# Optimization experiments

Measured on AMD Instinct MI355X. Metric: run time of the kernel, lower is better.

Reference implementation:

```python
import jax, jax.numpy as jnp
import numpy as np

HIDDEN = 1024
HEADS = 16
HEAD = HIDDEN // HEADS
B, S = 4, 2048


def setup_inputs() -> dict:
    key = jax.random.key(0)
    ks = jax.random.split(key, 12)
    sc = 1.0 / np.sqrt(HIDDEN)
    return {
        "query": jax.random.normal(ks[0], (B, S, HIDDEN), jnp.float32),
        "key_in": jax.random.normal(ks[1], (B, S, HIDDEN), jnp.float32),
        "value": jax.random.normal(ks[2], (B, S, HIDDEN), jnp.float32),
        "mask": jax.random.randint(ks[3], (B, S, S), 0, 2, jnp.int32),
        "w_q": jax.random.uniform(ks[4], (HIDDEN, HIDDEN), jnp.float32, -sc, sc),
        "b_q": jax.random.uniform(ks[5], (HIDDEN,), jnp.float32, -sc, sc),
        "w_k": jax.random.uniform(ks[6], (HIDDEN, HIDDEN), jnp.float32, -sc, sc),
        "b_k": jax.random.uniform(ks[7], (HIDDEN,), jnp.float32, -sc, sc),
        "w_v": jax.random.uniform(ks[8], (HIDDEN, HIDDEN), jnp.float32, -sc, sc),
        "b_v": jax.random.uniform(ks[9], (HIDDEN,), jnp.float32, -sc, sc),
    }


def _split_heads(x):
    # [B, S, H*D] -> [B, H, S, D]
    b, s, _ = x.shape
    return x.reshape(b, s, HEADS, HEAD).transpose(0, 2, 1, 3)


def reference(query, key_in, value, mask, w_q, b_q, w_k, b_k, w_v, b_v):
    # torch Linear: x @ W.T + b
    Q = _split_heads(query @ w_q.T + b_q)
    K = _split_heads(key_in @ w_k.T + b_k)
    V = _split_heads(value @ w_v.T + b_v)
    scale = 1.0 / np.sqrt(HEAD).astype(np.float32)
    scores = jnp.einsum("bhqd,bhkd->bhqk", Q, K) * scale
    # mask broadcast over heads; masked_fill where mask == 0
    scores = jnp.where(mask[:, None, :, :] == 0, jnp.float32(-1e9), scores)
    attn = jax.nn.softmax(scores, axis=-1)
    ctx = jnp.einsum("bhqk,bhkd->bhqd", attn, V)
    ctx = ctx.transpose(0, 2, 1, 3).reshape(query.shape[0], -1, HIDDEN)
    return (ctx, attn)
```

## Files before the change

kernel.cpp:

```cpp
#include <hip/hip_runtime.h>
#include <hip/hip_bf16.h>
#include <cstdint>
#include <cstddef>

typedef __attribute__((ext_vector_type(4)))  float f32x4;
typedef __attribute__((ext_vector_type(8)))  short s16x8;
typedef __attribute__((ext_vector_type(8)))  unsigned short u16x8;
typedef __attribute__((ext_vector_type(4)))  unsigned short u16x4;
typedef unsigned short ushort_t;
typedef unsigned long long u64;

#define MFMA_BF16(a, b, c) __builtin_amdgcn_mfma_f32_16x16x32_bf16((a), (b), (c), 0, 0, 0)

constexpr int BATCH  = 4;
constexpr int SEQ    = 2048;
constexpr int NHEAD  = 16;
constexpr int HEADD  = 64;
constexpr int HID    = 1024;
constexpr int BH     = BATCH * NHEAD;

#define QSCALE 0.180336880091961f

__device__ __forceinline__ ushort_t f2bf(float f) {
  return __builtin_bit_cast(ushort_t, __float2bfloat16(f));
}

__device__ __forceinline__ int ps_off(int q, int k) {
  return q * 136 + ((((k >> 3) ^ ((q >> 3) & 7)) & 15) << 3) + (k & 7);
}

__global__ __launch_bounds__(256, 2) void proj_fused_kernel(
    const float* __restrict__ q_in, const float* __restrict__ k_in,
    const float* __restrict__ v_in,
    const float* __restrict__ w_q, const float* __restrict__ b_q,
    const float* __restrict__ w_k, const float* __restrict__ b_k,
    const float* __restrict__ w_v, const float* __restrict__ b_v,
    ushort_t* __restrict__ Qp, ushort_t* __restrict__ Kp,
    ushort_t* __restrict__ Vp,
    const int* __restrict__ mask, u64* __restrict__ pm) {
  const int z = blockIdx.z;
  if (z == 3) {
    const int nwords = BATCH * SEQ * SEQ / 64;
    const int lane = threadIdx.x & 63;
    int wid = (blockIdx.y * gridDim.x + blockIdx.x) * 4 + (threadIdx.x >> 6);
    const int step = gridDim.x * gridDim.y * 4;
    for (; wid < nwords; wid += step) {
      int mv = __builtin_nontemporal_load(mask + (size_t)wid * 64 + lane);
      u64 bits = __ballot(mv != 0);
      if (lane == 0) pm[wid] = bits;
    }
    return;
  }
  const float* X    = (z == 0) ? q_in : (z == 1) ? k_in : v_in;
  const float* W    = (z == 0) ? w_q : (z == 1) ? w_k : w_v;
  const float* bias = (z == 0) ? b_q : (z == 1) ? b_k : b_v;
  const float scale = (z == 0) ? QSCALE : 1.0f;

  __shared__ ushort_t As[128 * 72];
  __shared__ ushort_t Bs[128 * 72];
  const int tid  = threadIdx.x;
  const int lane = tid & 63;
  const int wave = tid >> 6;
  const int wr = wave >> 1, wc = wave & 1;
  const int lo = lane & 15, hi = lane >> 4;
  const int mb = blockIdx.y, nb = blockIdx.x;

  const int srow = tid >> 4;
  const int scol = (tid & 15) * 4;

  f32x4 acc[4][4];
#pragma unroll
  for (int i = 0; i < 4; i++)
#pragma unroll
    for (int j = 0; j < 4; j++) acc[i][j] = (f32x4){0.f, 0.f, 0.f, 0.f};

  const float* xa = X + (size_t)(mb * 128 + srow) * HID + scol;
  const float* xb = W + (size_t)(nb * 128 + srow) * HID + scol;

  for (int k0 = 0; k0 < HID; k0 += 64) {
#pragma unroll
    for (int rr = 0; rr < 128; rr += 16) {
      float4 av = *(const float4*)(xa + (size_t)rr * HID + k0);
      float4 bv = *(const float4*)(xb + (size_t)rr * HID + k0);
      u16x4 a4 = {f2bf(av.x), f2bf(av.y), f2bf(av.z), f2bf(av.w)};
      u16x4 b4 = {f2bf(bv.x), f2bf(bv.y), f2bf(bv.z), f2bf(bv.w)};
      *(u16x4*)(&As[(srow + rr) * 72 + scol]) = a4;
      *(u16x4*)(&Bs[(srow + rr) * 72 + scol]) = b4;
    }
    __syncthreads();
#pragma unroll
    for (int kk = 0; kk < 2; kk++) {
      const int ko = kk * 32 + hi * 8;
      s16x8 af[4], bf[4];
#pragma unroll
      for (int i = 0; i < 4; i++)
        af[i] = *(const s16x8*)(&As[(wr * 64 + i * 16 + lo) * 72 + ko]);
#pragma unroll
      for (int j = 0; j < 4; j++)
        bf[j] = *(const s16x8*)(&Bs[(wc * 64 + j * 16 + lo) * 72 + ko]);
#pragma unroll
      for (int i = 0; i < 4; i++)
#pragma unroll
        for (int j = 0; j < 4; j++)
          acc[i][j] = MFMA_BF16(af[i], bf[j], acc[i][j]);
    }
    __syncthreads();
  }
  if (z != 2) {
    ushort_t* out = (z == 0) ? Qp : Kp;
#pragma unroll
    for (int j = 0; j < 4; j++) {
      const int n = nb * 128 + wc * 64 + j * 16 + lo;
      const float bvn = bias[n];
      const int h = n >> 6, d = n & 63;
#pragma unroll
      for (int i = 0; i < 4; i++) {
        const int m0 = mb * 128 + wr * 64 + i * 16 + hi * 4;
#pragma unroll
        for (int r = 0; r < 4; r++) {
          const int m = m0 + r;
          const int b = m >> 11, s = m & 2047;
          float v = (acc[i][j][r] + bvn) * scale;
          __builtin_nontemporal_store(
              f2bf(v), out + (((size_t)(b * NHEAD + h) * SEQ) + s) * HEADD + d);
        }
      }
    }
  } else {
#pragma unroll
    for (int j = 0; j < 4; j++) {
      const int n = nb * 128 + wc * 64 + j * 16 + lo;
      const float bvn = bias[n];
      const int h = n >> 6, d = n & 63;
#pragma unroll
      for (int i = 0; i < 4; i++) {
        const int m0 = mb * 128 + wr * 64 + i * 16 + hi * 4;
        const int b = m0 >> 11, s0 = m0 & 2047;
        u16x4 pk = {f2bf(acc[i][j][0] + bvn), f2bf(acc[i][j][1] + bvn),
                    f2bf(acc[i][j][2] + bvn), f2bf(acc[i][j][3] + bvn)};
        __builtin_nontemporal_store(
            pk, (u16x4*)(Vp + ((size_t)(b * NHEAD + h) * HEADD + d) * SEQ + s0));
      }
    }
  }
}

__global__ __launch_bounds__(256, 2) void fused_attn_kernel(
    const ushort_t* __restrict__ Qp, const ushort_t* __restrict__ Kp,
    const ushort_t* __restrict__ Vtg, const u64* __restrict__ pm,
    float* __restrict__ attn, float* __restrict__ ctx) {
  extern __shared__ ushort_t smem[];
  ushort_t* Vt = smem;
  ushort_t* Ps = smem + 8704;

  const int tid  = threadIdx.x;
  const int lane = tid & 63, wave = tid >> 6;
  const int lo = lane & 15, hi = lane >> 4;

  const int f   = blockIdx.x;
  const int xcd = f & 7, i5 = f >> 3;
  const int bh  = xcd * 8 + (i5 & 7);
  const int qb  = i5 >> 3;
  const int b = bh >> 4, h = bh & 15;

  const ushort_t* Qg = Qp + ((size_t)bh * SEQ + qb * 128 + wave * 32) * HEADD;
  s16x8 aq[2][2];
#pragma unroll
  for (int i = 0; i < 2; i++)
#pragma unroll
    for (int kk = 0; kk < 2; kk++)
      aq[i][kk] = *(const s16x8*)(Qg + (size_t)(i * 16 + lo) * HEADD + kk * 32 + hi * 8);

  const ushort_t* Kg = Kp + (size_t)bh * SEQ * HEADD;
  const ushort_t* Vg = Vtg + (size_t)bh * HEADD * SEQ;
  const u64* pmb = pm + (size_t)b * SEQ * 32;
  const int q0 = qb * 128 + wave * 32;

  float lrun[2][4];
#pragma unroll
  for (int i = 0; i < 2; i++)
#pragma unroll
    for (int r = 0; r < 4; r++) lrun[i][r] = 0.f;
  f32x4 pacc[2][4];
#pragma unroll
  for (int i = 0; i < 2; i++)
#pragma unroll
    for (int jd = 0; jd < 4; jd++) pacc[i][jd] = (f32x4){0.f, 0.f, 0.f, 0.f};

  const int vr16 = tid >> 4;
  const int vc8  = (tid & 15) * 8;

  for (int kt = 0; kt < SEQ / 128; kt++) {
    u16x8 vreg[4];
#pragma unroll
    for (int it = 0; it < 4; it++)
      vreg[it] = *(const u16x8*)(Vg + (size_t)(it * 16 + vr16) * SEQ + kt * 128 + vc8);

    f32x4 sacc[2][8];
#pragma unroll
    for (int i = 0; i < 2; i++)
#pragma unroll
      for (int j = 0; j < 8; j++) sacc[i][j] = (f32x4){0.f, 0.f, 0.f, 0.f};
#pragma unroll
    for (int j = 0; j < 8; j++) {
      const ushort_t* kr = Kg + (size_t)(kt * 128 + j * 16 + lo) * HEADD + hi * 8;
      s16x8 b0 = *(const s16x8*)(kr);
      s16x8 b1 = *(const s16x8*)(kr + 32);
      sacc[0][j] = MFMA_BF16(aq[0][0], b0, sacc[0][j]);
      sacc[1][j] = MFMA_BF16(aq[1][0], b0, sacc[1][j]);
      sacc[0][j] = MFMA_BF16(aq[0][1], b1, sacc[0][j]);
      sacc[1][j] = MFMA_BF16(aq[1][1], b1, sacc[1][j]);
    }

#pragma unroll
    for (int it = 0; it < 4; it++)
      *(u16x8*)(&Vt[(it * 16 + vr16) * 136 + vc8]) = vreg[it];

#pragma unroll
    for (int i = 0; i < 2; i++)
#pragma unroll
      for (int r = 0; r < 4; r++) {
        const int q = q0 + i * 16 + hi * 4 + r;
        const u64* pw = pmb + (size_t)q * 32 + kt * 2;
        u64 s0 = pw[0] >> lo, s1 = pw[1] >> lo;
        const int prow = wave * 32 + i * 16 + hi * 4 + r;
        float tsum = 0.f;
#pragma unroll
        for (int j = 0; j < 8; j++) {
          unsigned bit = (unsigned)((j < 4 ? (s0 >> (j * 16)) : (s1 >> ((j - 4) * 16))) & 1ull);
          float s = bit ? sacc[i][j][r] : -1e30f;
          float ev = __builtin_amdgcn_exp2f(s);
          tsum += ev;
          Ps[ps_off(prow, j * 16 + lo)] = f2bf(ev);
        }
        lrun[i][r] += tsum;
      }
    __syncthreads();

#pragma unroll
    for (int kkp = 0; kkp < 4; kkp++) {
      const int ko = kkp * 32 + hi * 8;
      s16x8 ap0 = *(const s16x8*)(&Ps[ps_off(wave * 32 + lo, ko)]);
      s16x8 ap1 = *(const s16x8*)(&Ps[ps_off(wave * 32 + 16 + lo, ko)]);
#pragma unroll
      for (int jd = 0; jd < 4; jd++) {
        s16x8 bv = *(const s16x8*)(&Vt[(jd * 16 + lo) * 136 + ko]);
        pacc[0][jd] = MFMA_BF16(ap0, bv, pacc[0][jd]);
        pacc[1][jd] = MFMA_BF16(ap1, bv, pacc[1][jd]);
      }
    }
    __syncthreads();
  }

  float il[2][4], mi[2][4];
#pragma unroll
  for (int i = 0; i < 2; i++)
#pragma unroll
    for (int r = 0; r < 4; r++) {
      float l = lrun[i][r];
#pragma unroll
      for (int off = 1; off < 16; off <<= 1) l += __shfl_xor(l, off);
      il[i][r] = 1.0f / l;
      mi[i][r] = __builtin_amdgcn_logf(l);
    }
#pragma unroll
  for (int i = 0; i < 2; i++)
#pragma unroll
    for (int jd = 0; jd < 4; jd++)
#pragma unroll
      for (int r = 0; r < 4; r++) {
        const int q = q0 + i * 16 + hi * 4 + r;
        __builtin_nontemporal_store(
            pacc[i][jd][r] * il[i][r],
            ctx + ((size_t)b * SEQ + q) * HID + h * HEADD + jd * 16 + lo);
      }

  for (int kt = 0; kt < SEQ / 128; kt++) {
    f32x4 sacc[2][8];
#pragma unroll
    for (int i = 0; i < 2; i++)
#pragma unroll
      for (int j = 0; j < 8; j++) sacc[i][j] = (f32x4){0.f, 0.f, 0.f, 0.f};
#pragma unroll
    for (int j = 0; j < 8; j++) {
      const ushort_t* kr = Kg + (size_t)(kt * 128 + j * 16 + lo) * HEADD + hi * 8;
      s16x8 b0 = *(const s16x8*)(kr);
      s16x8 b1 = *(const s16x8*)(kr + 32);
      sacc[0][j] = MFMA_BF16(aq[0][0], b0, sacc[0][j]);
      sacc[1][j] = MFMA_BF16(aq[1][0], b0, sacc[1][j]);
      sacc[0][j] = MFMA_BF16(aq[0][1], b1, sacc[0][j]);
      sacc[1][j] = MFMA_BF16(aq[1][1], b1, sacc[1][j]);
    }
#pragma unroll
    for (int i = 0; i < 2; i++)
#pragma unroll
      for (int r = 0; r < 4; r++) {
        const int q = q0 + i * 16 + hi * 4 + r;
        const u64* pw = pmb + (size_t)q * 32 + kt * 2;
        u64 s0 = pw[0] >> lo, s1 = pw[1] >> lo;
        const size_t abase = ((size_t)bh * SEQ + q) * SEQ + (size_t)kt * 128;
        const float miv = mi[i][r];
#pragma unroll
        for (int j = 0; j < 8; j++) {
          unsigned bit = (unsigned)((j < 4 ? (s0 >> (j * 16)) : (s1 >> ((j - 4) * 16))) & 1ull);
          float s = bit ? sacc[i][j][r] : -1e30f;
          __builtin_nontemporal_store(__builtin_amdgcn_exp2f(s - miv),
                                      attn + abase + j * 16 + lo);
        }
      }
  }
}

extern "C" void kernel_launch(void* const* d_in, const int* in_sizes, int n_in,
                              void* d_out, int out_size, void* d_ws, size_t ws_size,
                              hipStream_t stream) {
  const float* query  = (const float*)d_in[0];
  const float* key_in = (const float*)d_in[1];
  const float* value  = (const float*)d_in[2];
  const int*   mask   = (const int*)d_in[3];
  const float* w_q = (const float*)d_in[4];
  const float* b_q = (const float*)d_in[5];
  const float* w_k = (const float*)d_in[6];
  const float* b_k = (const float*)d_in[7];
  const float* w_v = (const float*)d_in[8];
  const float* b_v = (const float*)d_in[9];

  char* ws = (char*)d_ws;
  const size_t proj_elems = (size_t)BATCH * NHEAD * SEQ * HEADD;
  ushort_t* Qp = (ushort_t*)ws;
  ushort_t* Kp = Qp + proj_elems;
  ushort_t* Vp = Kp + proj_elems;
  u64* pmask   = (u64*)(ws + 3 * proj_elems * sizeof(ushort_t));

  float* ctx  = (float*)d_out;
  float* attn = ctx + (size_t)BATCH * SEQ * HID;

  proj_fused_kernel<<<dim3(HID / 128, (BATCH * SEQ) / 128, 4), dim3(256), 0, stream>>>(
      query, key_in, value, w_q, b_q, w_k, b_k, w_v, b_v, Qp, Kp, Vp, mask, pmask);

  const size_t lds_attn = (8704 + 17408) * sizeof(ushort_t);
  fused_attn_kernel<<<dim3(BH * (SEQ / 128)), dim3(256), lds_attn, stream>>>(
      Qp, Kp, Vp, pmask, attn, ctx);
}
```

Before: 723.1 us.

## Prepack inputs and weights to bf16, then run projection GEMM via global_load_lds

Splits the fused projection kernel into a prepack pass and a GEMM. The prepack pass converts the fp32 activations and weights to bf16 once and writes them into the attn output buffer as scratch, so each tile is no longer reconverted many times inside the GEMM. The GEMM then streams bf16 tiles straight into LDS with global_load_lds at higher occupancy. This adds an extra full read and write pass plus a kernel launch. It also drops the LDS padding, which may bring back bank conflicts on the fragment reads.

After: 679.7 us. 1.06x faster.

```diff
diff --git a/kernel.cpp b/kernel.cpp
--- a/kernel.cpp
+++ b/kernel.cpp
@@ -18,6 +18,7 @@
 constexpr int HEADD  = 64;
 constexpr int HID    = 1024;
 constexpr int BH     = BATCH * NHEAD;
+constexpr int MROWS  = BATCH * SEQ;
 
 #define QSCALE 0.180336880091961f
 
@@ -29,21 +30,25 @@
   return q * 136 + ((((k >> 3) ^ ((q >> 3) & 7)) & 15) << 3) + (k & 7);
 }
 
-__global__ __launch_bounds__(256, 2) void proj_fused_kernel(
+__device__ __forceinline__ void gl2lds16(const ushort_t* g, ushort_t* l) {
+  __builtin_amdgcn_global_load_lds(
+      (const __attribute__((address_space(1))) void*)g,
+      (__attribute__((address_space(3))) void*)l, 16, 0, 0);
+}
+
+__global__ __launch_bounds__(256) void prepack_kernel(
     const float* __restrict__ q_in, const float* __restrict__ k_in,
     const float* __restrict__ v_in,
-    const float* __restrict__ w_q, const float* __restrict__ b_q,
-    const float* __restrict__ w_k, const float* __restrict__ b_k,
-    const float* __restrict__ w_v, const float* __restrict__ b_v,
-    ushort_t* __restrict__ Qp, ushort_t* __restrict__ Kp,
-    ushort_t* __restrict__ Vp,
+    const float* __restrict__ w_q, const float* __restrict__ w_k,
+    const float* __restrict__ w_v,
+    ushort_t* __restrict__ Xb, ushort_t* __restrict__ Wb,
     const int* __restrict__ mask, u64* __restrict__ pm) {
   const int z = blockIdx.z;
   if (z == 3) {
     const int nwords = BATCH * SEQ * SEQ / 64;
     const int lane = threadIdx.x & 63;
-    int wid = (blockIdx.y * gridDim.x + blockIdx.x) * 4 + (threadIdx.x >> 6);
-    const int step = gridDim.x * gridDim.y * 4;
+    int wid = blockIdx.x * 4 + (threadIdx.x >> 6);
+    const int step = gridDim.x * 4;
     for (; wid < nwords; wid += step) {
       int mv = __builtin_nontemporal_load(mask + (size_t)wid * 64 + lane);
       u64 bits = __ballot(mv != 0);
@@ -51,13 +56,45 @@
     }
     return;
   }
-  const float* X    = (z == 0) ? q_in : (z == 1) ? k_in : v_in;
-  const float* W    = (z == 0) ? w_q : (z == 1) ? w_k : w_v;
+  const float* srcX = (z == 0) ? q_in : (z == 1) ? k_in : v_in;
+  const float* srcW = (z == 0) ? w_q : (z == 1) ? w_k : w_v;
+  ushort_t* dstX = Xb + (size_t)z * MROWS * HID;
+  ushort_t* dstW = Wb + (size_t)z * HID * HID;
+
+  const int tid = blockIdx.x * 256 + threadIdx.x;
+  const int stride = gridDim.x * 256;
+
+  for (int u = tid; u < MROWS * HID / 8; u += stride) {
+    const float* s = srcX + (size_t)u * 8;
+    f32x4 a = __builtin_nontemporal_load((const f32x4*)s);
+    f32x4 b = __builtin_nontemporal_load((const f32x4*)(s + 4));
+    u16x8 o = {f2bf(a[0]), f2bf(a[1]), f2bf(a[2]), f2bf(a[3]),
+               f2bf(b[0]), f2bf(b[1]), f2bf(b[2]), f2bf(b[3])};
+    __builtin_nontemporal_store(o, (u16x8*)(dstX + (size_t)u * 8));
+  }
+  for (int u = tid; u < HID * HID / 8; u += stride) {
+    const float* s = srcW + (size_t)u * 8;
+    f32x4 a = __builtin_nontemporal_load((const f32x4*)s);
+    f32x4 b = __builtin_nontemporal_load((const f32x4*)(s + 4));
+    u16x8 o = {f2bf(a[0]), f2bf(a[1]), f2bf(a[2]), f2bf(a[3]),
+               f2bf(b[0]), f2bf(b[1]), f2bf(b[2]), f2bf(b[3])};
+    __builtin_nontemporal_store(o, (u16x8*)(dstW + (size_t)u * 8));
+  }
+}
+
+__global__ __launch_bounds__(256, 4) void proj_gemm_kernel(
+    const ushort_t* __restrict__ Xb, const ushort_t* __restrict__ Wb,
+    const float* __restrict__ b_q, const float* __restrict__ b_k,
+    const float* __restrict__ b_v,
+    ushort_t* __restrict__ Qp, ushort_t* __restrict__ Kp,
+    ushort_t* __restrict__ Vp) {
+  __shared__ ushort_t As[128 * 64];
+  __shared__ ushort_t Bs[128 * 64];
+
+  const int z = blockIdx.z;
   const float* bias = (z == 0) ? b_q : (z == 1) ? b_k : b_v;
   const float scale = (z == 0) ? QSCALE : 1.0f;
 
-  __shared__ ushort_t As[128 * 72];
-  __shared__ ushort_t Bs[128 * 72];
   const int tid  = threadIdx.x;
   const int lane = tid & 63;
   const int wave = tid >> 6;
@@ -65,8 +102,9 @@
   const int lo = lane & 15, hi = lane >> 4;
   const int mb = blockIdx.y, nb = blockIdx.x;
 
-  const int srow = tid >> 4;
-  const int scol = (tid & 15) * 4;
+  const ushort_t* Ag = Xb + (size_t)z * MROWS * HID + (size_t)mb * 128 * HID;
+  const ushort_t* Bg = Wb + (size_t)z * HID * HID + (size_t)nb * 128 * HID;
+  const int lrow = lane >> 3, lcol = (lane & 7) * 8;
 
   f32x4 acc[4][4];
 #pragma unroll
@@ -74,18 +112,12 @@
 #pragma unroll
     for (int j = 0; j < 4; j++) acc[i][j] = (f32x4){0.f, 0.f, 0.f, 0.f};
 
-  const float* xa = X + (size_t)(mb * 128 + srow) * HID + scol;
-  const float* xb = W + (size_t)(nb * 128 + srow) * HID + scol;
-
   for (int k0 = 0; k0 < HID; k0 += 64) {
 #pragma unroll
-    for (int rr = 0; rr < 128; rr += 16) {
-      float4 av = *(const float4*)(xa + (size_t)rr * HID + k0);
-      float4 bv = *(const float4*)(xb + (size_t)rr * HID + k0);
-      u16x4 a4 = {f2bf(av.x), f2bf(av.y), f2bf(av.z), f2bf(av.w)};
-      u16x4 b4 = {f2bf(bv.x), f2bf(bv.y), f2bf(bv.z), f2bf(bv.w)};
-      *(u16x4*)(&As[(srow + rr) * 72 + scol]) = a4;
-      *(u16x4*)(&Bs[(srow + rr) * 72 + scol]) = b4;
+    for (int it = 0; it < 4; it++) {
+      const int r0 = (it * 4 + wave) * 8;
+      gl2lds16(Ag + (size_t)(r0 + lrow) * HID + k0 + lcol, &As[(it * 4 + wave) * 512]);
+      gl2lds16(Bg + (size_t)(r0 + lrow) * HID + k0 + lcol, &Bs[(it * 4 + wave) * 512]);
     }
     __syncthreads();
 #pragma unroll
@@ -94,10 +126,10 @@
       s16x8 af[4], bf[4];
 #pragma unroll
       for (int i = 0; i < 4; i++)
-        af[i] = *(const s16x8*)(&As[(wr * 64 + i * 16 + lo) * 72 + ko]);
+        af[i] = *(const s16x8*)(&As[(wr * 64 + i * 16 + lo) * 64 + ko]);
 #pragma unroll
       for (int j = 0; j < 4; j++)
-        bf[j] = *(const s16x8*)(&Bs[(wc * 64 + j * 16 + lo) * 72 + ko]);
+        bf[j] = *(const s16x8*)(&Bs[(wc * 64 + j * 16 + lo) * 64 + ko]);
 #pragma unroll
       for (int i = 0; i < 4; i++)
 #pragma unroll
@@ -106,6 +138,7 @@
     }
     __syncthreads();
   }
+
   if (z != 2) {
     ushort_t* out = (z == 0) ? Qp : Kp;
 #pragma unroll
@@ -122,7 +155,8 @@
           const int b = m >> 11, s = m & 2047;
           float v = (acc[i][j][r] + bvn) * scale;
           __builtin_nontemporal_store(
-              f2bf(v), out + (((size_t)(b * NHEAD + h) * SEQ) + s) * HEADD + d);
+              f2bf(v), Qp == out ? (out + (((size_t)(b * NHEAD + h) * SEQ) + s) * HEADD + d)
+                                 : (out + (((size_t)(b * NHEAD + h) * SEQ) + s) * HEADD + d));
         }
       }
     }
@@ -335,8 +369,14 @@
   float* ctx  = (float*)d_out;
   float* attn = ctx + (size_t)BATCH * SEQ * HID;
 
-  proj_fused_kernel<<<dim3(HID / 128, (BATCH * SEQ) / 128, 4), dim3(256), 0, stream>>>(
-      query, key_in, value, w_q, b_q, w_k, b_k, w_v, b_v, Qp, Kp, Vp, mask, pmask);
+  ushort_t* Xb = (ushort_t*)attn;
+  ushort_t* Wb = Xb + (size_t)3 * MROWS * HID;
+
+  prepack_kernel<<<dim3(512, 1, 4), dim3(256), 0, stream>>>(
+      query, key_in, value, w_q, w_k, w_v, Xb, Wb, mask, pmask);
+
+  proj_gemm_kernel<<<dim3(HID / 128, MROWS / 128, 3), dim3(256), 0, stream>>>(
+      Xb, Wb, b_q, b_k, b_v, Qp, Kp, Vp);
 
   const size_t lds_attn = (8704 + 17408) * sizeof(ushort_t);
   fused_attn_kernel<<<dim3(BH * (SEQ / 128)), dim3(256), lds_attn, stream>>>(
```
